# Kernel tuning notes

Hardware: AMD Instinct MI355X
Metric: run time of the kernel (lower is better)

Reference implementation:

```python
import jax, jax.numpy as jnp
import numpy as np

B, D, L = 8192, 2048, 4


def setup_inputs() -> dict:
    key = jax.random.key(0)
    kx, kw = jax.random.split(key)
    x = jax.random.normal(kx, (B, D), dtype=jnp.float32)
    # truncated_normal(stddev=0.01) approximated by scaled normal
    W = jax.random.normal(kw, (L, D), dtype=jnp.float32) * 0.01
    b = jnp.zeros((L, D), dtype=jnp.float32)
    return {"x": x, "W": W, "b": b}


def reference(x, W, b):
    # DCN cross layers. The original materializes the (B, d, d) outer product
    # o[b,j,k] = cross[b,j] * x0[b,k], multiplies by W[i] (broadcast over k)
    # and sums over j with keepdims. That reduces exactly to
    #   (sum_j cross[b,j]) * x0[b,k] * W[i,k]
    # so we compute the fused O(B*d) form (same math, no d^2 intermediate).
    x0 = x
    cross = x
    for i in range(W.shape[0]):
        s = jnp.sum(cross, axis=1, keepdims=True)        # (B, 1)
        cross = s * x0 * W[i] + b[i] + cross             # (B, d)
    return cross  # Flatten of (B, d) is identity
```

## Files before the change

kernel.cpp:

```cpp
#include <hip/hip_runtime.h>


constexpr int Bn = 8192;
constexpr int D = 2048;
constexpr int L = 4;
constexpr int THREADS = 256;
constexpr int VEC = 4;
constexpr int PASSES = D / (THREADS * VEC);
constexpr int RPB = 4;
constexpr int GRID = Bn / RPB;

__global__ __launch_bounds__(THREADS) void cross_layer_kernel(
    const float* __restrict__ x,
    const float* __restrict__ W,
    const float* __restrict__ b,
    float* __restrict__ out)
{
    const int tid = threadIdx.x;
    const int lane = tid & 63;
    const int wid = tid >> 6;

    __shared__ float red[4][8];

    float4 wv[L][PASSES];
    float4 bs[PASSES];
    float bred[3];
    bred[0] = bred[1] = bred[2] = 0.f;

#pragma unroll
    for (int p = 0; p < PASSES; ++p) {
        const int d = p * (THREADS * VEC) + tid * VEC;
        float4 bsum = make_float4(0.f, 0.f, 0.f, 0.f);
#pragma unroll
        for (int i = 0; i < L; ++i) {
            wv[i][p] = *reinterpret_cast<const float4*>(W + i * D + d);
            float4 bb = *reinterpret_cast<const float4*>(b + i * D + d);
            bsum.x += bb.x; bsum.y += bb.y; bsum.z += bb.z; bsum.w += bb.w;
            if (i < 3) bred[i] += bb.x + bb.y + bb.z + bb.w;
        }
        bs[p] = bsum;
    }

#pragma unroll
    for (int k = 0; k < 3; ++k) {
#pragma unroll
        for (int off = 32; off > 0; off >>= 1)
            bred[k] += __shfl_down(bred[k], off, 64);
    }
    if (lane == 0) {
#pragma unroll
        for (int k = 0; k < 3; ++k) red[wid][k] = bred[k];
    }
    __syncthreads();
    float Bsc[3];
#pragma unroll
    for (int k = 0; k < 3; ++k)
        Bsc[k] = red[0][k] + red[1][k] + red[2][k] + red[3][k];

    float4 xv[PASSES], xn[PASSES];
    {
        const float* xr = x + (size_t)blockIdx.x * D;
#pragma unroll
        for (int p = 0; p < PASSES; ++p)
            xv[p] = *reinterpret_cast<const float4*>(xr + p * (THREADS * VEC) + tid * VEC);
    }

    for (int k = 0; k < RPB; ++k) {
        if (k + 1 < RPB) {
            const float* xr = x + (size_t)(blockIdx.x + GRID * (k + 1)) * D;
#pragma unroll
            for (int p = 0; p < PASSES; ++p)
                xn[p] = *reinterpret_cast<const float4*>(xr + p * (THREADS * VEC) + tid * VEC);
        }

        float sm[4];
        sm[0] = sm[1] = sm[2] = sm[3] = 0.f;
#pragma unroll
        for (int p = 0; p < PASSES; ++p) {
            sm[0] += xv[p].x + xv[p].y + xv[p].z + xv[p].w;
#pragma unroll
            for (int i = 0; i < 3; ++i) {
                sm[1 + i] += xv[p].x * wv[i][p].x + xv[p].y * wv[i][p].y
                           + xv[p].z * wv[i][p].z + xv[p].w * wv[i][p].w;
            }
        }
#pragma unroll
        for (int q = 0; q < 4; ++q) {
#pragma unroll
            for (int off = 32; off > 0; off >>= 1)
                sm[q] += __shfl_down(sm[q], off, 64);
        }
        __syncthreads();
        if (lane == 0) {
#pragma unroll
            for (int q = 0; q < 4; ++q) red[wid][q] = sm[q];
        }
        __syncthreads();

        const float T  = red[0][0] + red[1][0] + red[2][0] + red[3][0];
        float A[3];
#pragma unroll
        for (int q = 0; q < 3; ++q)
            A[q] = red[0][1 + q] + red[1][1 + q] + red[2][1 + q] + red[3][1 + q];

        float s[L];
        s[0] = T;
#pragma unroll
        for (int i = 1; i < L; ++i)
            s[i] = s[i - 1] * (1.f + A[i - 1]) + Bsc[i - 1];

        float* outr = out + (size_t)(blockIdx.x + GRID * k) * D;
#pragma unroll
        for (int p = 0; p < PASSES; ++p) {
            float cx = 1.f, cy = 1.f, cz = 1.f, cw = 1.f;
#pragma unroll
            for (int i = 0; i < L; ++i) {
                cx += s[i] * wv[i][p].x;
                cy += s[i] * wv[i][p].y;
                cz += s[i] * wv[i][p].z;
                cw += s[i] * wv[i][p].w;
            }
            float4 o;
            o.x = xv[p].x * cx + bs[p].x;
            o.y = xv[p].y * cy + bs[p].y;
            o.z = xv[p].z * cz + bs[p].z;
            o.w = xv[p].w * cw + bs[p].w;
            *reinterpret_cast<float4*>(outr + p * (THREADS * VEC) + tid * VEC) = o;
        }

#pragma unroll
        for (int p = 0; p < PASSES; ++p) xv[p] = xn[p];
    }
}

extern "C" void kernel_launch(void* const* d_in, const int* in_sizes, int n_in,
                              void* d_out, int out_size, void* d_ws, size_t ws_size,
                              hipStream_t stream) {
    const float* x = (const float*)d_in[0];
    const float* W = (const float*)d_in[1];
    const float* b = (const float*)d_in[2];
    float* out = (float*)d_out;
    cross_layer_kernel<<<GRID, THREADS, 0, stream>>>(x, W, b, out);
}
```

Baseline: 27.90 us.

## Batch two rows per iteration with nontemporal loads/stores and double-buffered reduction

Each block now processes two rows per iteration (two iterations of two rows instead of four single-row steps), so one block reduction covers eight partial sums. This halves the number of reductions and barriers per block. The shared reduction buffer is double-buffered by iteration parity, which removes the leading __syncthreads before each write. Loads of x and stores of out use nontemporal builtins to avoid polluting cache with streamed data. In exchange, register pressure rises with two rows in flight plus the prefetch buffers, which can lower occupancy.

```diff
diff --git a/kernel.cpp b/kernel.cpp
--- a/kernel.cpp
+++ b/kernel.cpp
@@ -1,5 +1,7 @@
 #include <hip/hip_runtime.h>
 
+
+typedef float v4 __attribute__((ext_vector_type(4)));
 
 constexpr int Bn = 8192;
 constexpr int D = 2048;
@@ -7,8 +9,18 @@
 constexpr int THREADS = 256;
 constexpr int VEC = 4;
 constexpr int PASSES = D / (THREADS * VEC);
-constexpr int RPB = 4;
+constexpr int RPI = 2;
+constexpr int ITERS = 2;
+constexpr int RPB = RPI * ITERS;
 constexpr int GRID = Bn / RPB;
+
+__device__ inline v4 ntload(const float* p) {
+    return __builtin_nontemporal_load(reinterpret_cast<const v4*>(p));
+}
+__device__ inline void ntstore(float* p, v4 v) {
+    __builtin_nontemporal_store(v, reinterpret_cast<v4*>(p));
+}
+__device__ inline float hsum(v4 v) { return v.x + v.y + v.z + v.w; }
 
 __global__ __launch_bounds__(THREADS) void cross_layer_kernel(
     const float* __restrict__ x,
@@ -20,116 +32,125 @@
     const int lane = tid & 63;
     const int wid = tid >> 6;
 
-    __shared__ float red[4][8];
+    __shared__ float redp[4][3];
+    __shared__ float red[2][4][2 * 4];
 
-    float4 wv[L][PASSES];
-    float4 bs[PASSES];
-    float bred[3];
-    bred[0] = bred[1] = bred[2] = 0.f;
+    v4 wv[L][PASSES];
+    v4 bs[PASSES];
+    float bred[3] = {0.f, 0.f, 0.f};
 
 #pragma unroll
     for (int p = 0; p < PASSES; ++p) {
         const int d = p * (THREADS * VEC) + tid * VEC;
-        float4 bsum = make_float4(0.f, 0.f, 0.f, 0.f);
+        v4 bsum = {0.f, 0.f, 0.f, 0.f};
 #pragma unroll
         for (int i = 0; i < L; ++i) {
-            wv[i][p] = *reinterpret_cast<const float4*>(W + i * D + d);
-            float4 bb = *reinterpret_cast<const float4*>(b + i * D + d);
-            bsum.x += bb.x; bsum.y += bb.y; bsum.z += bb.z; bsum.w += bb.w;
-            if (i < 3) bred[i] += bb.x + bb.y + bb.z + bb.w;
+            wv[i][p] = *reinterpret_cast<const v4*>(W + i * D + d);
+            v4 bb = *reinterpret_cast<const v4*>(b + i * D + d);
+            bsum += bb;
+            if (i < 3) bred[i] += hsum(bb);
         }
         bs[p] = bsum;
     }
 
 #pragma unroll
-    for (int k = 0; k < 3; ++k) {
+    for (int k = 0; k < 3; ++k)
 #pragma unroll
         for (int off = 32; off > 0; off >>= 1)
             bred[k] += __shfl_down(bred[k], off, 64);
-    }
-    if (lane == 0) {
+    if (lane == 0)
 #pragma unroll
-        for (int k = 0; k < 3; ++k) red[wid][k] = bred[k];
-    }
+        for (int k = 0; k < 3; ++k) redp[wid][k] = bred[k];
     __syncthreads();
     float Bsc[3];
 #pragma unroll
     for (int k = 0; k < 3; ++k)
-        Bsc[k] = red[0][k] + red[1][k] + red[2][k] + red[3][k];
+        Bsc[k] = redp[0][k] + redp[1][k] + redp[2][k] + redp[3][k];
 
-    float4 xv[PASSES], xn[PASSES];
+    v4 xv[RPI][PASSES], xn[RPI][PASSES];
     {
-        const float* xr = x + (size_t)blockIdx.x * D;
+        const int col = tid * VEC;
 #pragma unroll
-        for (int p = 0; p < PASSES; ++p)
-            xv[p] = *reinterpret_cast<const float4*>(xr + p * (THREADS * VEC) + tid * VEC);
+        for (int r = 0; r < RPI; ++r) {
+            const float* xr = x + (size_t)(blockIdx.x + GRID * r) * D;
+#pragma unroll
+            for (int p = 0; p < PASSES; ++p)
+                xv[r][p] = ntload(xr + p * (THREADS * VEC) + col);
+        }
     }
 
-    for (int k = 0; k < RPB; ++k) {
-        if (k + 1 < RPB) {
-            const float* xr = x + (size_t)(blockIdx.x + GRID * (k + 1)) * D;
 #pragma unroll
-            for (int p = 0; p < PASSES; ++p)
-                xn[p] = *reinterpret_cast<const float4*>(xr + p * (THREADS * VEC) + tid * VEC);
+    for (int it = 0; it < ITERS; ++it) {
+        if (it + 1 < ITERS) {
+            const int col = tid * VEC;
+#pragma unroll
+            for (int r = 0; r < RPI; ++r) {
+                const float* xr = x + (size_t)(blockIdx.x + GRID * (RPI * (it + 1) + r)) * D;
+#pragma unroll
+                for (int p = 0; p < PASSES; ++p)
+                    xn[r][p] = ntload(xr + p * (THREADS * VEC) + col);
+            }
         }
 
-        float sm[4];
-        sm[0] = sm[1] = sm[2] = sm[3] = 0.f;
+        float sm[RPI * 4];
 #pragma unroll
-        for (int p = 0; p < PASSES; ++p) {
-            sm[0] += xv[p].x + xv[p].y + xv[p].z + xv[p].w;
+        for (int q = 0; q < RPI * 4; ++q) sm[q] = 0.f;
 #pragma unroll
-            for (int i = 0; i < 3; ++i) {
-                sm[1 + i] += xv[p].x * wv[i][p].x + xv[p].y * wv[i][p].y
-                           + xv[p].z * wv[i][p].z + xv[p].w * wv[i][p].w;
+        for (int r = 0; r < RPI; ++r)
+#pragma unroll
+            for (int p = 0; p < PASSES; ++p) {
+                sm[r * 4 + 0] += hsum(xv[r][p]);
+#pragma unroll
+                for (int i = 0; i < 3; ++i)
+                    sm[r * 4 + 1 + i] += hsum(xv[r][p] * wv[i][p]);
             }
-        }
+
 #pragma unroll
-        for (int q = 0; q < 4; ++q) {
+        for (int q = 0; q < RPI * 4; ++q)
 #pragma unroll
             for (int off = 32; off > 0; off >>= 1)
                 sm[q] += __shfl_down(sm[q], off, 64);
-        }
-        __syncthreads();
-        if (lane == 0) {
+
+        if (lane == 0)
 #pragma unroll
-            for (int q = 0; q < 4; ++q) red[wid][q] = sm[q];
-        }
+            for (int q = 0; q < RPI * 4; ++q) red[it & 1][wid][q] = sm[q];
         __syncthreads();
 
-        const float T  = red[0][0] + red[1][0] + red[2][0] + red[3][0];
-        float A[3];
+        float s[RPI][L];
 #pragma unroll
-        for (int q = 0; q < 3; ++q)
-            A[q] = red[0][1 + q] + red[1][1 + q] + red[2][1 + q] + red[3][1 + q];
+        for (int r = 0; r < RPI; ++r) {
+            const float T  = red[it & 1][0][r * 4] + red[it & 1][1][r * 4]
+                           + red[it & 1][2][r * 4] + red[it & 1][3][r * 4];
+            float A[3];
+#pragma unroll
+            for (int q = 0; q < 3; ++q)
+                A[q] = red[it & 1][0][r * 4 + 1 + q] + red[it & 1][1][r * 4 + 1 + q]
+                     + red[it & 1][2][r * 4 + 1 + q] + red[it & 1][3][r * 4 + 1 + q];
+            s[r][0] = T;
+#pragma unroll
+            for (int i = 1; i < L; ++i)
+                s[r][i] = s[r][i - 1] * (1.f + A[i - 1]) + Bsc[i - 1];
+        }
 
-        float s[L];
-        s[0] = T;
+        const int col = tid * VEC;
 #pragma unroll
-        for (int i = 1; i < L; ++i)
-            s[i] = s[i - 1] * (1.f + A[i - 1]) + Bsc[i - 1];
-
-        float* outr = out + (size_t)(blockIdx.x + GRID * k) * D;
+        for (int r = 0; r < RPI; ++r) {
+            float* outr = out + (size_t)(blockIdx.x + GRID * (RPI * it + r)) * D;
 #pragma unroll
-        for (int p = 0; p < PASSES; ++p) {
-            float cx = 1.f, cy = 1.f, cz = 1.f, cw = 1.f;
+            for (int p = 0; p < PASSES; ++p) {
+                v4 c = {1.f, 1.f, 1.f, 1.f};
 #pragma unroll
-            for (int i = 0; i < L; ++i) {
-                cx += s[i] * wv[i][p].x;
-                cy += s[i] * wv[i][p].y;
-                cz += s[i] * wv[i][p].z;
-                cw += s[i] * wv[i][p].w;
+                for (int i = 0; i < L; ++i)
+                    c += s[r][i] * wv[i][p];
+                ntstore(outr + p * (THREADS * VEC) + col, xv[r][p] * c + bs[p]);
             }
-            float4 o;
-            o.x = xv[p].x * cx + bs[p].x;
-            o.y = xv[p].y * cy + bs[p].y;
-            o.z = xv[p].z * cz + bs[p].z;
-            o.w = xv[p].w * cw + bs[p].w;
-            *reinterpret_cast<float4*>(outr + p * (THREADS * VEC) + tid * VEC) = o;
         }
 
 #pragma unroll
-        for (int p = 0; p < PASSES; ++p) xv[p] = xn[p];
+        for (int r = 0; r < RPI; ++r)
+#pragma unroll
+            for (int p = 0; p < PASSES; ++p)
+                xv[r][p] = xn[r][p];
     }
 }
 
```

After: 30.26 us. 8.5% more time.
